# Kernel optimization log

Measured on AMD Instinct MI355X. Metric: run time of the kernel, lower is better.

## Reference

```python
import jax, jax.numpy as jnp
import numpy as np

EPS_COS = 1e-8   # nxn_cos_sim eps
SMOOTH = 1e-4    # DiceLoss smooth
EPS_DICE = 1e-7  # smp soft_dice_score clamp_min eps

BS, C, H, W = 8, 512, 128, 128
K = 512  # codebook / num classes


def setup_inputs() -> dict:
    key = jax.random.key(0)
    k1, k2, k3 = jax.random.split(key, 3)
    output = jax.random.normal(k1, (BS, C, H, W), dtype=jnp.float32)
    embeddings = jax.random.normal(k2, (K, C), dtype=jnp.float32)
    # ground-truth one-hot annotation (bs, K, h, w)
    gt_labels = jax.random.randint(k3, (BS, H, W), 0, K)
    ann_one_hot = jax.nn.one_hot(gt_labels, K, dtype=jnp.float32).transpose(0, 3, 1, 2)
    return {"output": output, "ann_one_hot": ann_one_hot, "embeddings": embeddings}


def reference(output, ann_one_hot, embeddings):
    bs, c, h, w = output.shape
    k = embeddings.shape[0]
    x = output.transpose(0, 2, 3, 1).reshape(-1, c)           # [N, C]
    # nxn cosine similarity [N, K]
    numerator = x @ embeddings.T
    a_l2 = jnp.sum(x * x, axis=1)                              # [N]
    b_l2 = jnp.sum(embeddings * embeddings, axis=1)            # [K]
    denominator = jnp.maximum(jnp.sqrt(a_l2[:, None] * b_l2[None, :]), EPS_COS)
    labels = jnp.argmax(numerator / denominator, axis=-1).reshape(bs, h, w)
    # ann_to_one_hot -> (bs, K, h, w)
    pred_one_hot = jax.nn.one_hot(labels, k, dtype=output.dtype).transpose(0, 3, 1, 2)
    # smp DiceLoss(mode='multilabel', smooth=1e-4, from_logits=False)
    yp = pred_one_hot.reshape(bs, k, -1)
    yt = ann_one_hot.reshape(bs, k, -1).astype(yp.dtype)
    dims = (0, 2)
    intersection = jnp.sum(yp * yt, axis=dims)                 # [K]
    cardinality = jnp.sum(yp + yt, axis=dims)                  # [K]
    score = (2.0 * intersection + SMOOTH) / jnp.maximum(cardinality + SMOOTH, EPS_DICE)
    loss = 1.0 - score
    present = (jnp.sum(yt, axis=dims) > 0).astype(loss.dtype)  # only classes present in GT
    return jnp.mean(loss * present)
```

## Files before the change

kernel.cpp:

```cpp
#include <hip/hip_runtime.h>
#include <hip/hip_bf16.h>

#define BSZ 8
#define CDIM 512
#define KDIM 512
#define HWSZ 16384
#define NPIX (BSZ*HWSZ)

#define ROWU 20

using bf16x8 = __attribute__((ext_vector_type(8))) short;
using f32x4  = __attribute__((ext_vector_type(4))) float;

__global__ __launch_bounds__(64) void prep_emb_kernel(const float* __restrict__ E,
                                                      unsigned short* __restrict__ Eb) {
  int k = blockIdx.x;
  int lane = threadIdx.x;
  const float4* row = (const float4*)(E + (size_t)k * CDIM);
  float4 v0 = row[lane * 2], v1 = row[lane * 2 + 1];
  float ss = v0.x*v0.x + v0.y*v0.y + v0.z*v0.z + v0.w*v0.w
           + v1.x*v1.x + v1.y*v1.y + v1.z*v1.z + v1.w*v1.w;
  #pragma unroll
  for (int d = 1; d < 64; d <<= 1) ss += __shfl_xor(ss, d, 64);
  float rinv = rsqrtf(fmaxf(ss, 1e-24f));
  float f[8] = {v0.x, v0.y, v0.z, v0.w, v1.x, v1.y, v1.z, v1.w};
  unsigned o[8];
  #pragma unroll
  for (int e = 0; e < 8; ++e) {
    float x = f[e] * rinv;
    unsigned u = __builtin_bit_cast(unsigned, x);
    o[e] = (u + 0x7FFFu + ((u >> 16) & 1u)) >> 16;
  }
  uint4 pack;
  pack.x = o[0] | (o[1] << 16);
  pack.y = o[2] | (o[3] << 16);
  pack.z = o[4] | (o[5] << 16);
  pack.w = o[6] | (o[7] << 16);
  ((uint4*)(Eb + (size_t)k * CDIM))[lane] = pack;
}

__global__ __launch_bounds__(256) void gt_count_kernel(const float* __restrict__ ANN,
                                                       float* __restrict__ gt_count) {
  int slice = blockIdx.x;
  int k = slice & (KDIM - 1);
  const float4* p = (const float4*)(ANN + (size_t)slice * HWSZ);
  float s = 0.f;
  #pragma unroll
  for (int i = 0; i < 16; ++i) {
    float4 v = p[threadIdx.x + i * 256];
    s += v.x + v.y + v.z + v.w;
  }
  #pragma unroll
  for (int d = 1; d < 64; d <<= 1) s += __shfl_xor(s, d, 64);
  __shared__ float sw[4];
  if ((threadIdx.x & 63) == 0) sw[threadIdx.x >> 6] = s;
  __syncthreads();
  if (threadIdx.x == 0) {
    atomicAdd(&gt_count[k], sw[0] + sw[1] + sw[2] + sw[3]);
  }
}

__global__ __launch_bounds__(256, 2) void gemm_fused(
    const float* __restrict__ X, const float* __restrict__ ANN,
    const unsigned short* __restrict__ Eb,
    int* __restrict__ pred_count, int* __restrict__ inter) {
  __shared__ unsigned int lds[2][64 * ROWU];
  int tid  = threadIdx.x;
  int wv   = tid >> 6;
  int lane = tid & 63;
  int p15  = lane & 15, q = lane >> 4;
  int cp   = tid & 15;
  int pq   = tid >> 4;
  int px0  = blockIdx.x * 64;
  int b    = px0 >> 14;
  int hw   = px0 & (HWSZ - 1);

  const float*          Xs = X  + ((size_t)b * CDIM + 2 * cp) * HWSZ + hw + 4 * pq;
  const unsigned short* Er = Eb + (size_t)(wv * 128 + p15) * CDIM + q * 8;

  {
    float4 v0 = *(const float4*)Xs;
    float4 v1 = *(const float4*)(Xs + HWSZ);
    float f0[4] = {v0.x, v0.y, v0.z, v0.w};
    float f1[4] = {v1.x, v1.y, v1.z, v1.w};
    #pragma unroll
    for (int j = 0; j < 4; ++j) {
      unsigned u = (__builtin_bit_cast(unsigned, f0[j]) >> 16)
                 | (__builtin_bit_cast(unsigned, f1[j]) & 0xFFFF0000u);
      lds[0][(4 * pq + j) * ROWU + cp] = u;
    }
  }

  f32x4 acc[4][8];
  #pragma unroll
  for (int m = 0; m < 4; ++m)
    #pragma unroll
    for (int n = 0; n < 8; ++n)
      acc[m][n] = (f32x4){0.f, 0.f, 0.f, 0.f};

  for (int cs = 0; cs < 16; ++cs) {
    int cur = cs & 1;
    bf16x8 bb[8];
    #pragma unroll
    for (int n = 0; n < 8; ++n)
      bb[n] = *(const bf16x8*)(Er + (size_t)n * 16 * CDIM + cs * 32);
    float4 w0, w1;
    if (cs < 15) {
      const float* nsrc = Xs + (size_t)(cs + 1) * 32 * HWSZ;
      w0 = *(const float4*)nsrc;
      w1 = *(const float4*)(nsrc + HWSZ);
    }
    __syncthreads();
    bf16x8 a[4];
    #pragma unroll
    for (int m = 0; m < 4; ++m)
      a[m] = *(bf16x8*)&lds[cur][(m * 16 + p15) * ROWU + q * 4];
    #pragma unroll
    for (int n = 0; n < 8; ++n)
      #pragma unroll
      for (int m = 0; m < 4; ++m)
        acc[m][n] = __builtin_amdgcn_mfma_f32_16x16x32_bf16(a[m], bb[n], acc[m][n], 0, 0, 0);
    if (cs < 15) {
      float f0[4] = {w0.x, w0.y, w0.z, w0.w};
      float f1[4] = {w1.x, w1.y, w1.z, w1.w};
      #pragma unroll
      for (int j = 0; j < 4; ++j) {
        unsigned u = (__builtin_bit_cast(unsigned, f0[j]) >> 16)
                   | (__builtin_bit_cast(unsigned, f1[j]) & 0xFFFF0000u);
        lds[cur ^ 1][(4 * pq + j) * ROWU + cp] = u;
      }
    }
  }

  __shared__ float s_v[4][64];
  __shared__ int   s_k[4][64];
  #pragma unroll
  for (int m = 0; m < 4; ++m) {
    #pragma unroll
    for (int r = 0; r < 4; ++r) {
      float best = acc[m][0][r];
      int bn = 0;
      #pragma unroll
      for (int n = 1; n < 8; ++n) {
        float v = acc[m][n][r];
        if (v > best) { best = v; bn = n; }
      }
      int bk = wv * 128 + bn * 16 + p15;
      #pragma unroll
      for (int d = 1; d < 16; d <<= 1) {
        float ov = __shfl_xor(best, d, 64);
        int   ok = __shfl_xor(bk, d, 64);
        if (ov > best || (ov == best && ok < bk)) { best = ov; bk = ok; }
      }
      if (p15 == 0) {
        int p = m * 16 + q * 4 + r;
        s_v[wv][p] = best;
        s_k[wv][p] = bk;
      }
    }
  }
  __syncthreads();
  if (tid < 64) {
    int p = tid;
    float best = s_v[0][p]; int bk = s_k[0][p];
    #pragma unroll
    for (int w = 1; w < 4; ++w) {
      float v = s_v[w][p]; int kk = s_k[w][p];
      if (v > best || (v == best && kk < bk)) { best = v; bk = kk; }
    }
    atomicAdd(&pred_count[bk], 1);
    float g = ANN[((size_t)b * KDIM + bk) * HWSZ + hw + p];
    if (g > 0.5f) atomicAdd(&inter[bk], 1);
  }
}

__global__ __launch_bounds__(512) void final_kernel(
    const int* __restrict__ pred_count, const int* __restrict__ inter,
    const float* __restrict__ gt_count, float* __restrict__ out) {
  int k = threadIdx.x;
  float G = gt_count[k];
  float P = (float)pred_count[k];
  float I = (float)inter[k];
  float card  = P + G;
  float score = (2.f * I + 1e-4f) / fmaxf(card + 1e-4f, 1e-7f);
  float v = (G > 0.f) ? (1.f - score) : 0.f;
  #pragma unroll
  for (int d = 1; d < 64; d <<= 1) v += __shfl_xor(v, d, 64);
  __shared__ float sw[8];
  if ((k & 63) == 0) sw[k >> 6] = v;
  __syncthreads();
  if (k == 0) {
    float s = 0.f;
    #pragma unroll
    for (int i = 0; i < 8; ++i) s += sw[i];
    out[0] = s / (float)KDIM;
  }
}

extern "C" void kernel_launch(void* const* d_in, const int* in_sizes, int n_in,
                              void* d_out, int out_size, void* d_ws, size_t ws_size,
                              hipStream_t stream) {
  const float* X   = (const float*)d_in[0];
  const float* ANN = (const float*)d_in[1];
  const float* E   = (const float*)d_in[2];

  char* base = (char*)d_ws;
  unsigned short* Eb = (unsigned short*)base;
  float* gt_count    = (float*)(base + 524288);
  int*   pred_count  = (int*)  (base + 524288 + 2048);
  int*   inter       = (int*)  (base + 524288 + 4096);

  hipMemsetAsync(base + 524288, 0, 6144, stream);
  prep_emb_kernel<<<KDIM, 64, 0, stream>>>(E, Eb);
  gt_count_kernel<<<BSZ * KDIM, 256, 0, stream>>>(ANN, gt_count);
  gemm_fused<<<NPIX / 64, 256, 0, stream>>>(X, ANN, Eb, pred_count, inter);
  final_kernel<<<1, 512, 0, stream>>>(pred_count, inter, gt_count, (float*)d_out);
}
```

Measured before the change: 241.8 us.

## Fuse GT count reduction into GEMM kernel using extra waves per block

The separate gt_count kernel, which streams the whole 256MB one-hot annotation, is removed. Its reduction now runs inside the GEMM kernel on the upper 256 threads of a 512-thread block. Each block reads a 32768-float contiguous chunk of ANN and accumulates two class-slice partial sums via atomics, while the lower 256 threads keep staging X into LDS. Each wave now covers 64 codebook columns instead of 128, which cuts accumulator registers, and s_setprio raises MFMA priority. The aim is to overlap the annotation streaming with GEMM compute and save a launch, at the cost of more waves contending for bandwidth and a wider argmax merge across blocks.

```diff
diff --git a/kernel.cpp b/kernel.cpp
--- a/kernel.cpp
+++ b/kernel.cpp
@@ -39,46 +39,33 @@
   ((uint4*)(Eb + (size_t)k * CDIM))[lane] = pack;
 }
 
-__global__ __launch_bounds__(256) void gt_count_kernel(const float* __restrict__ ANN,
-                                                       float* __restrict__ gt_count) {
-  int slice = blockIdx.x;
-  int k = slice & (KDIM - 1);
-  const float4* p = (const float4*)(ANN + (size_t)slice * HWSZ);
-  float s = 0.f;
-  #pragma unroll
-  for (int i = 0; i < 16; ++i) {
-    float4 v = p[threadIdx.x + i * 256];
-    s += v.x + v.y + v.z + v.w;
-  }
-  #pragma unroll
-  for (int d = 1; d < 64; d <<= 1) s += __shfl_xor(s, d, 64);
-  __shared__ float sw[4];
-  if ((threadIdx.x & 63) == 0) sw[threadIdx.x >> 6] = s;
-  __syncthreads();
-  if (threadIdx.x == 0) {
-    atomicAdd(&gt_count[k], sw[0] + sw[1] + sw[2] + sw[3]);
-  }
-}
-
-__global__ __launch_bounds__(256, 2) void gemm_fused(
+__global__ __launch_bounds__(512, 4) void gemm_fused(
     const float* __restrict__ X, const float* __restrict__ ANN,
     const unsigned short* __restrict__ Eb,
+    float* __restrict__ gt_count,
     int* __restrict__ pred_count, int* __restrict__ inter) {
   __shared__ unsigned int lds[2][64 * ROWU];
+  __shared__ float s_v[8][64];
+  __shared__ int   s_k[8][64];
   int tid  = threadIdx.x;
   int wv   = tid >> 6;
   int lane = tid & 63;
   int p15  = lane & 15, q = lane >> 4;
-  int cp   = tid & 15;
-  int pq   = tid >> 4;
   int px0  = blockIdx.x * 64;
   int b    = px0 >> 14;
   int hw   = px0 & (HWSZ - 1);
 
-  const float*          Xs = X  + ((size_t)b * CDIM + 2 * cp) * HWSZ + hw + 4 * pq;
-  const unsigned short* Er = Eb + (size_t)(wv * 128 + p15) * CDIM + q * 8;
-
-  {
+  bool stager = (tid < 256);
+  int cp = tid & 15;
+  int pq = (tid >> 4) & 15;
+  const float* Xs = X + ((size_t)b * CDIM + 2 * cp) * HWSZ + hw + 4 * pq;
+
+  const float* Ap = ANN + (size_t)blockIdx.x * 32768 + (size_t)(tid & 255) * 4;
+  float annAcc0 = 0.f, annAcc1 = 0.f;
+
+  const unsigned short* Er = Eb + (size_t)(wv * 64 + p15) * CDIM + q * 8;
+
+  if (stager) {
     float4 v0 = *(const float4*)Xs;
     float4 v1 = *(const float4*)(Xs + HWSZ);
     float f0[4] = {v0.x, v0.y, v0.z, v0.w};
@@ -91,49 +78,71 @@
     }
   }
 
-  f32x4 acc[4][8];
+  f32x4 acc[4][4];
   #pragma unroll
   for (int m = 0; m < 4; ++m)
     #pragma unroll
-    for (int n = 0; n < 8; ++n)
+    for (int n = 0; n < 4; ++n)
       acc[m][n] = (f32x4){0.f, 0.f, 0.f, 0.f};
 
   for (int cs = 0; cs < 16; ++cs) {
     int cur = cs & 1;
-    bf16x8 bb[8];
-    #pragma unroll
-    for (int n = 0; n < 8; ++n)
+    bf16x8 bb[4];
+    #pragma unroll
+    for (int n = 0; n < 4; ++n)
       bb[n] = *(const bf16x8*)(Er + (size_t)n * 16 * CDIM + cs * 32);
     float4 w0, w1;
-    if (cs < 15) {
-      const float* nsrc = Xs + (size_t)(cs + 1) * 32 * HWSZ;
-      w0 = *(const float4*)nsrc;
-      w1 = *(const float4*)(nsrc + HWSZ);
+    if (stager) {
+      if (cs < 15) {
+        const float* nsrc = Xs + (size_t)(cs + 1) * 32 * HWSZ;
+        w0 = *(const float4*)nsrc;
+        w1 = *(const float4*)(nsrc + HWSZ);
+      }
+    } else {
+      w0 = *(const float4*)(Ap + cs * 2048);
+      w1 = *(const float4*)(Ap + cs * 2048 + 1024);
     }
     __syncthreads();
     bf16x8 a[4];
     #pragma unroll
     for (int m = 0; m < 4; ++m)
       a[m] = *(bf16x8*)&lds[cur][(m * 16 + p15) * ROWU + q * 4];
-    #pragma unroll
-    for (int n = 0; n < 8; ++n)
+    __builtin_amdgcn_s_setprio(1);
+    #pragma unroll
+    for (int n = 0; n < 4; ++n)
       #pragma unroll
       for (int m = 0; m < 4; ++m)
         acc[m][n] = __builtin_amdgcn_mfma_f32_16x16x32_bf16(a[m], bb[n], acc[m][n], 0, 0, 0);
-    if (cs < 15) {
-      float f0[4] = {w0.x, w0.y, w0.z, w0.w};
-      float f1[4] = {w1.x, w1.y, w1.z, w1.w};
-      #pragma unroll
-      for (int j = 0; j < 4; ++j) {
-        unsigned u = (__builtin_bit_cast(unsigned, f0[j]) >> 16)
-                   | (__builtin_bit_cast(unsigned, f1[j]) & 0xFFFF0000u);
-        lds[cur ^ 1][(4 * pq + j) * ROWU + cp] = u;
-      }
-    }
-  }
-
-  __shared__ float s_v[4][64];
-  __shared__ int   s_k[4][64];
+    __builtin_amdgcn_s_setprio(0);
+    if (stager) {
+      if (cs < 15) {
+        float f0[4] = {w0.x, w0.y, w0.z, w0.w};
+        float f1[4] = {w1.x, w1.y, w1.z, w1.w};
+        #pragma unroll
+        for (int j = 0; j < 4; ++j) {
+          unsigned u = (__builtin_bit_cast(unsigned, f0[j]) >> 16)
+                     | (__builtin_bit_cast(unsigned, f1[j]) & 0xFFFF0000u);
+          lds[cur ^ 1][(4 * pq + j) * ROWU + cp] = u;
+        }
+      }
+    } else {
+      float s = (w0.x + w0.y) + (w0.z + w0.w) + (w1.x + w1.y) + (w1.z + w1.w);
+      if (cs < 8) annAcc0 += s; else annAcc1 += s;
+    }
+  }
+
+  if (!stager) {
+    #pragma unroll
+    for (int d = 1; d < 64; d <<= 1) {
+      annAcc0 += __shfl_xor(annAcc0, d, 64);
+      annAcc1 += __shfl_xor(annAcc1, d, 64);
+    }
+    if (lane == 0) {
+      atomicAdd(&gt_count[(blockIdx.x * 2)     & (KDIM - 1)], annAcc0);
+      atomicAdd(&gt_count[(blockIdx.x * 2 + 1) & (KDIM - 1)], annAcc1);
+    }
+  }
+
   #pragma unroll
   for (int m = 0; m < 4; ++m) {
     #pragma unroll
@@ -141,11 +150,11 @@
       float best = acc[m][0][r];
       int bn = 0;
       #pragma unroll
-      for (int n = 1; n < 8; ++n) {
+      for (int n = 1; n < 4; ++n) {
         float v = acc[m][n][r];
         if (v > best) { best = v; bn = n; }
       }
-      int bk = wv * 128 + bn * 16 + p15;
+      int bk = wv * 64 + bn * 16 + p15;
       #pragma unroll
       for (int d = 1; d < 16; d <<= 1) {
         float ov = __shfl_xor(best, d, 64);
@@ -164,7 +173,7 @@
     int p = tid;
     float best = s_v[0][p]; int bk = s_k[0][p];
     #pragma unroll
-    for (int w = 1; w < 4; ++w) {
+    for (int w = 1; w < 8; ++w) {
       float v = s_v[w][p]; int kk = s_k[w][p];
       if (v > best || (v == best && kk < bk)) { best = v; bk = kk; }
     }
@@ -212,7 +221,6 @@
 
   hipMemsetAsync(base + 524288, 0, 6144, stream);
   prep_emb_kernel<<<KDIM, 64, 0, stream>>>(E, Eb);
-  gt_count_kernel<<<BSZ * KDIM, 256, 0, stream>>>(ANN, gt_count);
-  gemm_fused<<<NPIX / 64, 256, 0, stream>>>(X, ANN, Eb, pred_count, inter);
+  gemm_fused<<<NPIX / 64, 512, 0, stream>>>(X, ANN, Eb, gt_count, pred_count, inter);
   final_kernel<<<1, 512, 0, stream>>>(pred_count, inter, gt_count, (float*)d_out);
 }
```

After: 315.5 us. 30.5% more time.

## Fuse GT count reduction into GEMM kernel and double K-chunk per barrier

Applied to the files above, without the earlier changes.

Drops the separate gt_count kernel: each GEMM block now also sums two 16384-float annotation slices and atomically adds them into gt_count, so the 268MB annotation read overlaps with GEMM work instead of running as its own pass. The GEMM main loop is also restructured to stage 64 channels per LDS buffer (ROWU widened to 36), halving the number of barriers. This adds register and LDS pressure and up-front memory traffic in each GEMM block, which could hurt occupancy.

```diff
diff --git a/kernel.cpp b/kernel.cpp
--- a/kernel.cpp
+++ b/kernel.cpp
@@ -7,10 +7,15 @@
 #define HWSZ 16384
 #define NPIX (BSZ*HWSZ)
 
-#define ROWU 20
+#define ROWU 36
 
 using bf16x8 = __attribute__((ext_vector_type(8))) short;
 using f32x4  = __attribute__((ext_vector_type(4))) float;
+
+__device__ __forceinline__ unsigned pack2bf16(float lo, float hi) {
+  return (__builtin_bit_cast(unsigned, lo) >> 16) |
+         (__builtin_bit_cast(unsigned, hi) & 0xFFFF0000u);
+}
 
 __global__ __launch_bounds__(64) void prep_emb_kernel(const float* __restrict__ E,
                                                       unsigned short* __restrict__ Eb) {
@@ -39,32 +44,14 @@
   ((uint4*)(Eb + (size_t)k * CDIM))[lane] = pack;
 }
 
-__global__ __launch_bounds__(256) void gt_count_kernel(const float* __restrict__ ANN,
-                                                       float* __restrict__ gt_count) {
-  int slice = blockIdx.x;
-  int k = slice & (KDIM - 1);
-  const float4* p = (const float4*)(ANN + (size_t)slice * HWSZ);
-  float s = 0.f;
-  #pragma unroll
-  for (int i = 0; i < 16; ++i) {
-    float4 v = p[threadIdx.x + i * 256];
-    s += v.x + v.y + v.z + v.w;
-  }
-  #pragma unroll
-  for (int d = 1; d < 64; d <<= 1) s += __shfl_xor(s, d, 64);
-  __shared__ float sw[4];
-  if ((threadIdx.x & 63) == 0) sw[threadIdx.x >> 6] = s;
-  __syncthreads();
-  if (threadIdx.x == 0) {
-    atomicAdd(&gt_count[k], sw[0] + sw[1] + sw[2] + sw[3]);
-  }
-}
-
 __global__ __launch_bounds__(256, 2) void gemm_fused(
     const float* __restrict__ X, const float* __restrict__ ANN,
     const unsigned short* __restrict__ Eb,
+    float* __restrict__ gt_count,
     int* __restrict__ pred_count, int* __restrict__ inter) {
   __shared__ unsigned int lds[2][64 * ROWU];
+  __shared__ float s_v[4][64];
+  __shared__ int   s_k[4][64];
   int tid  = threadIdx.x;
   int wv   = tid >> 6;
   int lane = tid & 63;
@@ -75,19 +62,41 @@
   int b    = px0 >> 14;
   int hw   = px0 & (HWSZ - 1);
 
+  {
+    const float* Ap = ANN + (size_t)blockIdx.x * 32768 + tid * 4;
+    float s0 = 0.f, s1 = 0.f;
+    #pragma unroll
+    for (int r = 0; r < 16; ++r) {
+      float4 u = *(const float4*)(Ap + (size_t)r * 1024);
+      float4 v = *(const float4*)(Ap + 16384 + (size_t)r * 1024);
+      s0 += (u.x + u.y) + (u.z + u.w);
+      s1 += (v.x + v.y) + (v.z + v.w);
+    }
+    #pragma unroll
+    for (int d = 1; d < 64; d <<= 1) {
+      s0 += __shfl_xor(s0, d, 64);
+      s1 += __shfl_xor(s1, d, 64);
+    }
+    if (lane == 0) {
+      atomicAdd(&gt_count[(blockIdx.x * 2)     & (KDIM - 1)], s0);
+      atomicAdd(&gt_count[(blockIdx.x * 2 + 1) & (KDIM - 1)], s1);
+    }
+  }
+
   const float*          Xs = X  + ((size_t)b * CDIM + 2 * cp) * HWSZ + hw + 4 * pq;
   const unsigned short* Er = Eb + (size_t)(wv * 128 + p15) * CDIM + q * 8;
 
   {
-    float4 v0 = *(const float4*)Xs;
-    float4 v1 = *(const float4*)(Xs + HWSZ);
-    float f0[4] = {v0.x, v0.y, v0.z, v0.w};
-    float f1[4] = {v1.x, v1.y, v1.z, v1.w};
+    float4 w0 = *(const float4*)(Xs);
+    float4 w1 = *(const float4*)(Xs + HWSZ);
+    float4 w2 = *(const float4*)(Xs + 32 * HWSZ);
+    float4 w3 = *(const float4*)(Xs + 33 * HWSZ);
+    float f0[4] = {w0.x, w0.y, w0.z, w0.w}, f1[4] = {w1.x, w1.y, w1.z, w1.w};
+    float f2[4] = {w2.x, w2.y, w2.z, w2.w}, f3[4] = {w3.x, w3.y, w3.z, w3.w};
     #pragma unroll
     for (int j = 0; j < 4; ++j) {
-      unsigned u = (__builtin_bit_cast(unsigned, f0[j]) >> 16)
-                 | (__builtin_bit_cast(unsigned, f1[j]) & 0xFFFF0000u);
-      lds[0][(4 * pq + j) * ROWU + cp] = u;
+      lds[0][(4 * pq + j) * ROWU + cp]      = pack2bf16(f0[j], f1[j]);
+      lds[0][(4 * pq + j) * ROWU + 16 + cp] = pack2bf16(f2[j], f3[j]);
     }
   }
 
@@ -98,42 +107,45 @@
     for (int n = 0; n < 8; ++n)
       acc[m][n] = (f32x4){0.f, 0.f, 0.f, 0.f};
 
-  for (int cs = 0; cs < 16; ++cs) {
-    int cur = cs & 1;
-    bf16x8 bb[8];
-    #pragma unroll
-    for (int n = 0; n < 8; ++n)
-      bb[n] = *(const bf16x8*)(Er + (size_t)n * 16 * CDIM + cs * 32);
-    float4 w0, w1;
-    if (cs < 15) {
-      const float* nsrc = Xs + (size_t)(cs + 1) * 32 * HWSZ;
-      w0 = *(const float4*)nsrc;
-      w1 = *(const float4*)(nsrc + HWSZ);
+  #pragma unroll 2
+  for (int i = 0; i < 8; ++i) {
+    int cur = i & 1;
+    float4 w0, w1, w2, w3;
+    if (i < 7) {
+      const float* nx = Xs + (size_t)(i + 1) * 64 * HWSZ;
+      w0 = *(const float4*)(nx);
+      w1 = *(const float4*)(nx + HWSZ);
+      w2 = *(const float4*)(nx + 32 * HWSZ);
+      w3 = *(const float4*)(nx + 33 * HWSZ);
     }
     __syncthreads();
-    bf16x8 a[4];
-    #pragma unroll
-    for (int m = 0; m < 4; ++m)
-      a[m] = *(bf16x8*)&lds[cur][(m * 16 + p15) * ROWU + q * 4];
-    #pragma unroll
-    for (int n = 0; n < 8; ++n)
+    #pragma unroll
+    for (int h = 0; h < 2; ++h) {
+      bf16x8 bb[8];
+      #pragma unroll
+      for (int n = 0; n < 8; ++n)
+        bb[n] = *(const bf16x8*)(Er + (size_t)n * 16 * CDIM + i * 64 + h * 32);
+      bf16x8 a[4];
       #pragma unroll
       for (int m = 0; m < 4; ++m)
-        acc[m][n] = __builtin_amdgcn_mfma_f32_16x16x32_bf16(a[m], bb[n], acc[m][n], 0, 0, 0);
-    if (cs < 15) {
-      float f0[4] = {w0.x, w0.y, w0.z, w0.w};
-      float f1[4] = {w1.x, w1.y, w1.z, w1.w};
+        a[m] = *(bf16x8*)&lds[cur][(m * 16 + p15) * ROWU + h * 16 + q * 4];
+      #pragma unroll
+      for (int n = 0; n < 8; ++n)
+        #pragma unroll
+        for (int m = 0; m < 4; ++m)
+          acc[m][n] = __builtin_amdgcn_mfma_f32_16x16x32_bf16(a[m], bb[n], acc[m][n], 0, 0, 0);
+    }
+    if (i < 7) {
+      float f0[4] = {w0.x, w0.y, w0.z, w0.w}, f1[4] = {w1.x, w1.y, w1.z, w1.w};
+      float f2[4] = {w2.x, w2.y, w2.z, w2.w}, f3[4] = {w3.x, w3.y, w3.z, w3.w};
       #pragma unroll
       for (int j = 0; j < 4; ++j) {
-        unsigned u = (__builtin_bit_cast(unsigned, f0[j]) >> 16)
-                   | (__builtin_bit_cast(unsigned, f1[j]) & 0xFFFF0000u);
-        lds[cur ^ 1][(4 * pq + j) * ROWU + cp] = u;
-      }
-    }
-  }
-
-  __shared__ float s_v[4][64];
-  __shared__ int   s_k[4][64];
+        lds[cur ^ 1][(4 * pq + j) * ROWU + cp]      = pack2bf16(f0[j], f1[j]);
+        lds[cur ^ 1][(4 * pq + j) * ROWU + 16 + cp] = pack2bf16(f2[j], f3[j]);
+      }
+    }
+  }
+
   #pragma unroll
   for (int m = 0; m < 4; ++m) {
     #pragma unroll
@@ -212,7 +224,6 @@
 
   hipMemsetAsync(base + 524288, 0, 6144, stream);
   prep_emb_kernel<<<KDIM, 64, 0, stream>>>(E, Eb);
-  gt_count_kernel<<<BSZ * KDIM, 256, 0, stream>>>(ANN, gt_count);
-  gemm_fused<<<NPIX / 64, 256, 0, stream>>>(X, ANN, Eb, pred_count, inter);
+  gemm_fused<<<NPIX / 64, 256, 0, stream>>>(X, ANN, Eb, gt_count, pred_count, inter);
   final_kernel<<<1, 512, 0, stream>>>(pred_count, inter, gt_count, (float*)d_out);
 }
```

Result: slower. 256.9 us, median of 2 (+6.3%).

## Fuse GT counting into GEMM kernel via interleaved blocks and drop memset

Applied to the files above, without the earlier changes.

Merges the ground-truth counting kernel into the GEMM/argmax kernel by giving odd block IDs the annotation-reduction work, so the two streams of work run concurrently in one launch. The counter zeroing moves into the embedding prep kernel, replacing a separate memset. MFMA sections are also wrapped in raised wave priority. This removes launch gaps and tail idle time, but mixes heterogeneous blocks that compete for bandwidth and LDS.

```diff
diff --git a/kernel.cpp b/kernel.cpp
--- a/kernel.cpp
+++ b/kernel.cpp
@@ -12,10 +12,21 @@
 using bf16x8 = __attribute__((ext_vector_type(8))) short;
 using f32x4  = __attribute__((ext_vector_type(4))) float;
 
+__device__ __forceinline__ unsigned pack2bf16(float lo, float hi) {
+  return (__builtin_bit_cast(unsigned, lo) >> 16) |
+         (__builtin_bit_cast(unsigned, hi) & 0xFFFF0000u);
+}
+
 __global__ __launch_bounds__(64) void prep_emb_kernel(const float* __restrict__ E,
-                                                      unsigned short* __restrict__ Eb) {
+                                                      unsigned short* __restrict__ Eb,
+                                                      float* __restrict__ counters) {
   int k = blockIdx.x;
   int lane = threadIdx.x;
+  if (k == 0) {
+    uint4 z = {0u, 0u, 0u, 0u};
+    #pragma unroll
+    for (int j = 0; j < 6; ++j) ((uint4*)counters)[lane + 64 * j] = z;
+  }
   const float4* row = (const float4*)(E + (size_t)k * CDIM);
   float4 v0 = row[lane * 2], v1 = row[lane * 2 + 1];
   float ss = v0.x*v0.x + v0.y*v0.y + v0.z*v0.z + v0.w*v0.w
@@ -39,43 +50,55 @@
   ((uint4*)(Eb + (size_t)k * CDIM))[lane] = pack;
 }
 
-__global__ __launch_bounds__(256) void gt_count_kernel(const float* __restrict__ ANN,
-                                                       float* __restrict__ gt_count) {
-  int slice = blockIdx.x;
-  int k = slice & (KDIM - 1);
-  const float4* p = (const float4*)(ANN + (size_t)slice * HWSZ);
-  float s = 0.f;
-  #pragma unroll
-  for (int i = 0; i < 16; ++i) {
-    float4 v = p[threadIdx.x + i * 256];
-    s += v.x + v.y + v.z + v.w;
-  }
-  #pragma unroll
-  for (int d = 1; d < 64; d <<= 1) s += __shfl_xor(s, d, 64);
-  __shared__ float sw[4];
-  if ((threadIdx.x & 63) == 0) sw[threadIdx.x >> 6] = s;
-  __syncthreads();
-  if (threadIdx.x == 0) {
-    atomicAdd(&gt_count[k], sw[0] + sw[1] + sw[2] + sw[3]);
-  }
-}
-
-__global__ __launch_bounds__(256, 2) void gemm_fused(
+__global__ __launch_bounds__(256, 2) void fused_kernel(
     const float* __restrict__ X, const float* __restrict__ ANN,
     const unsigned short* __restrict__ Eb,
+    float* __restrict__ gt_count,
     int* __restrict__ pred_count, int* __restrict__ inter) {
   __shared__ unsigned int lds[2][64 * ROWU];
-  int tid  = threadIdx.x;
-  int wv   = tid >> 6;
+  __shared__ float s_v[4][64];
+  __shared__ int   s_k[4][64];
+  int tid = threadIdx.x;
+  int bid = blockIdx.x;
   int lane = tid & 63;
-  int p15  = lane & 15, q = lane >> 4;
-  int cp   = tid & 15;
-  int pq   = tid >> 4;
-  int px0  = blockIdx.x * 64;
-  int b    = px0 >> 14;
-  int hw   = px0 & (HWSZ - 1);
-
-  const float*          Xs = X  + ((size_t)b * CDIM + 2 * cp) * HWSZ + hw + 4 * pq;
+
+  if (bid & 1) {
+    int g = bid >> 1;
+    const float* A0 = ANN + (size_t)(2 * g) * HWSZ + 4 * tid;
+    float s0 = 0.f, s1 = 0.f;
+    #pragma unroll
+    for (int i = 0; i < 16; ++i) {
+      float4 u = *(const float4*)(A0 + (size_t)i * 1024);
+      float4 v = *(const float4*)(A0 + HWSZ + (size_t)i * 1024);
+      s0 += (u.x + u.y) + (u.z + u.w);
+      s1 += (v.x + v.y) + (v.z + v.w);
+    }
+    #pragma unroll
+    for (int d = 1; d < 64; d <<= 1) {
+      s0 += __shfl_xor(s0, d, 64);
+      s1 += __shfl_xor(s1, d, 64);
+    }
+    if (lane == 0) { s_v[tid >> 6][0] = s0; s_v[tid >> 6][1] = s1; }
+    __syncthreads();
+    if (tid == 0) {
+      atomicAdd(&gt_count[(2 * g) & (KDIM - 1)],
+                s_v[0][0] + s_v[1][0] + s_v[2][0] + s_v[3][0]);
+      atomicAdd(&gt_count[(2 * g + 1) & (KDIM - 1)],
+                s_v[0][1] + s_v[1][1] + s_v[2][1] + s_v[3][1]);
+    }
+    return;
+  }
+
+  int wv  = tid >> 6;
+  int p15 = lane & 15, q = lane >> 4;
+  int cpair = tid >> 4;
+  int px4   = tid & 15;
+  int pxblk = bid >> 1;
+  int px0 = pxblk * 64;
+  int b   = px0 >> 14;
+  int hw  = px0 & (HWSZ - 1);
+
+  const float*          Xs = X  + ((size_t)b * CDIM + 2 * cpair) * HWSZ + hw + 4 * px4;
   const unsigned short* Er = Eb + (size_t)(wv * 128 + p15) * CDIM + q * 8;
 
   {
@@ -84,11 +107,8 @@
     float f0[4] = {v0.x, v0.y, v0.z, v0.w};
     float f1[4] = {v1.x, v1.y, v1.z, v1.w};
     #pragma unroll
-    for (int j = 0; j < 4; ++j) {
-      unsigned u = (__builtin_bit_cast(unsigned, f0[j]) >> 16)
-                 | (__builtin_bit_cast(unsigned, f1[j]) & 0xFFFF0000u);
-      lds[0][(4 * pq + j) * ROWU + cp] = u;
-    }
+    for (int j = 0; j < 4; ++j)
+      lds[0][(4 * px4 + j) * ROWU + cpair] = pack2bf16(f0[j], f1[j]);
   }
 
   f32x4 acc[4][8];
@@ -115,25 +135,22 @@
     #pragma unroll
     for (int m = 0; m < 4; ++m)
       a[m] = *(bf16x8*)&lds[cur][(m * 16 + p15) * ROWU + q * 4];
+    __builtin_amdgcn_s_setprio(1);
     #pragma unroll
     for (int n = 0; n < 8; ++n)
       #pragma unroll
       for (int m = 0; m < 4; ++m)
         acc[m][n] = __builtin_amdgcn_mfma_f32_16x16x32_bf16(a[m], bb[n], acc[m][n], 0, 0, 0);
+    __builtin_amdgcn_s_setprio(0);
     if (cs < 15) {
       float f0[4] = {w0.x, w0.y, w0.z, w0.w};
       float f1[4] = {w1.x, w1.y, w1.z, w1.w};
       #pragma unroll
-      for (int j = 0; j < 4; ++j) {
-        unsigned u = (__builtin_bit_cast(unsigned, f0[j]) >> 16)
-                   | (__builtin_bit_cast(unsigned, f1[j]) & 0xFFFF0000u);
-        lds[cur ^ 1][(4 * pq + j) * ROWU + cp] = u;
-      }
-    }
-  }
-
-  __shared__ float s_v[4][64];
-  __shared__ int   s_k[4][64];
+      for (int j = 0; j < 4; ++j)
+        lds[cur ^ 1][(4 * px4 + j) * ROWU + cpair] = pack2bf16(f0[j], f1[j]);
+    }
+  }
+
   #pragma unroll
   for (int m = 0; m < 4; ++m) {
     #pragma unroll
@@ -210,9 +227,7 @@
   int*   pred_count  = (int*)  (base + 524288 + 2048);
   int*   inter       = (int*)  (base + 524288 + 4096);
 
-  hipMemsetAsync(base + 524288, 0, 6144, stream);
-  prep_emb_kernel<<<KDIM, 64, 0, stream>>>(E, Eb);
-  gt_count_kernel<<<BSZ * KDIM, 256, 0, stream>>>(ANN, gt_count);
-  gemm_fused<<<NPIX / 64, 256, 0, stream>>>(X, ANN, Eb, pred_count, inter);
+  prep_emb_kernel<<<KDIM, 64, 0, stream>>>(E, Eb, gt_count);
+  fused_kernel<<<4096, 256, 0, stream>>>(X, ANN, Eb, gt_count, pred_count, inter);
   final_kernel<<<1, 512, 0, stream>>>(pred_count, inter, gt_count, (float*)d_out);
 }
```

Result: slower. 313.4 us (+29.6%).
